# Performance work log

Measured on AMD Instinct MI355X. Metric: run time of the kernel, lower is better.

## Reference

```python
import jax, jax.numpy as jnp
import numpy as np

B, S, D, H, DK, DV = 4, 2048, 512, 8, 64, 64

def setup_inputs() -> dict:
    key = jax.random.key(0)
    ks = jax.random.split(key, 8)
    q = jax.random.normal(ks[0], (B, S, D), dtype=jnp.float32)
    k = jax.random.normal(ks[1], (B, S, D), dtype=jnp.float32)
    v = jax.random.normal(ks[2], (B, S, D), dtype=jnp.float32)
    mask = jax.random.uniform(ks[3], (B, 1, S, S), dtype=jnp.float32)
    sc = 1.0 / np.sqrt(D)
    Wq = jax.random.normal(ks[4], (D, H * DK), dtype=jnp.float32) * sc
    Wk = jax.random.normal(ks[5], (D, H * DK), dtype=jnp.float32) * sc
    Wv = jax.random.normal(ks[6], (D, H * DV), dtype=jnp.float32) * sc
    gamma = jnp.asarray(100.0, dtype=jnp.float32)
    return {"q": q, "k": k, "v": v, "mask": mask, "Wq": Wq, "Wk": Wk, "Wv": Wv, "gamma": gamma}

def reference(q, k, v, mask, Wq, Wk, Wv, gamma):
    temperature = jnp.asarray(DK ** 0.5, dtype=q.dtype)
    # project and split heads: [B,S,H,dk] -> [B,H,S,dk]
    qh = (q @ Wq).reshape(B, S, H, DK).transpose(0, 2, 1, 3)
    kh = (k @ Wk).reshape(B, S, H, DK).transpose(0, 2, 1, 3)
    vh = (v @ Wv).reshape(B, S, H, DV).transpose(0, 2, 1, 3)
    # scores [B,H,S,S] with learnable gamma-scaled additive mask
    scores = jnp.einsum('bhqd,bhkd->bhqk', qh / temperature, kh)
    scores = scores + mask * gamma
    attn = jax.nn.softmax(scores, axis=-1)  # dropout is identity in eval
    out = jnp.einsum('bhqk,bhkd->bhqd', attn, vh)
    out = out.transpose(0, 2, 1, 3).reshape(B, S, H * DV)
    return (out, attn)
```

## Files before the change

kernel.cpp:

```cpp
#include <hip/hip_runtime.h>

typedef __attribute__((ext_vector_type(8))) short short8;
typedef __attribute__((ext_vector_type(4))) float f32x4;

__device__ __forceinline__ short f2bf(float f) {
  union { float f; unsigned u; } x; x.f = f;
  return (short)((x.u + 0x7FFFu + ((x.u >> 16) & 1u)) >> 16);
}
__device__ __forceinline__ unsigned pk2(float a, float b) {
  return (unsigned)(unsigned short)f2bf(a) | ((unsigned)(unsigned short)f2bf(b) << 16);
}
__device__ __forceinline__ float bfu2f(unsigned lo16) {
  union { unsigned u; float f; } x; x.u = lo16 << 16; return x.f;
}

__global__ __launch_bounds__(256) void prep_wt_k(const float* __restrict__ Wq,
    const float* __restrict__ Wk, const float* __restrict__ Wv,
    short* __restrict__ wt) {
  int idx = blockIdx.x * 256 + threadIdx.x;
  int m = idx >> 18;
  int r = idx & 0x3FFFF;
  int k = r >> 9, n = r & 511;
  const float* W = (m == 0) ? Wq : (m == 1) ? Wk : Wv;
  wt[(m << 18) + (n << 9) + k] = f2bf(W[(k << 9) + n]);
}

__global__ __launch_bounds__(256) void xcvt_k(const float* __restrict__ q,
    const float* __restrict__ k_, const float* __restrict__ v,
    short* __restrict__ xb) {
  int i = blockIdx.x * 256 + threadIdx.x;
  int m = i >> 19;
  int r = i & 0x7FFFF;
  const float* X = (m == 0) ? q : (m == 1) ? k_ : v;
  float4 f0 = ((const float4*)X)[2 * r];
  float4 f1 = ((const float4*)X)[2 * r + 1];
  short8 t;
  t[0] = f2bf(f0.x); t[1] = f2bf(f0.y); t[2] = f2bf(f0.z); t[3] = f2bf(f0.w);
  t[4] = f2bf(f1.x); t[5] = f2bf(f1.y); t[6] = f2bf(f1.z); t[7] = f2bf(f1.w);
  *(short8*)(xb + (size_t)i * 8) = t;
}

template<int BF>
__global__ __launch_bounds__(64) void proj_k(const float* __restrict__ q,
    const float* __restrict__ k_, const float* __restrict__ v,
    const short* __restrict__ xb, const short* __restrict__ wt,
    short* __restrict__ qh, short* __restrict__ kh, short* __restrict__ vt) {
  int bid = blockIdx.x;
  int mat = bid >> 10;
  int t = bid & 1023;
  int tm = t >> 3, tn = t & 7;
  const float* X = (mat == 0) ? q : (mat == 1) ? k_ : v;
  const short* Xb = xb + ((size_t)mat << 22);
  const short* W = wt + ((size_t)mat << 18);
  int lane = threadIdx.x;
  int lr = lane & 15, lg = lane >> 4;
  int m0 = tm << 6, n0 = tn << 6;
  f32x4 acc[4][4];
  #pragma unroll
  for (int i = 0; i < 4; i++)
    #pragma unroll
    for (int j = 0; j < 4; j++) acc[i][j] = (f32x4){0.f, 0.f, 0.f, 0.f};
  for (int k0 = 0; k0 < 512; k0 += 32) {
    short8 a[4], bfr[4];
    #pragma unroll
    for (int i = 0; i < 4; i++) {
      if (BF) {
        a[i] = *(const short8*)(Xb + (size_t)(m0 + 16 * i + lr) * 512 + k0 + 8 * lg);
      } else {
        const float* p = X + (size_t)(m0 + 16 * i + lr) * 512 + k0 + 8 * lg;
        float4 f0 = *(const float4*)p;
        float4 f1 = *(const float4*)(p + 4);
        short8 tt;
        tt[0] = f2bf(f0.x); tt[1] = f2bf(f0.y); tt[2] = f2bf(f0.z); tt[3] = f2bf(f0.w);
        tt[4] = f2bf(f1.x); tt[5] = f2bf(f1.y); tt[6] = f2bf(f1.z); tt[7] = f2bf(f1.w);
        a[i] = tt;
      }
    }
    #pragma unroll
    for (int j = 0; j < 4; j++)
      bfr[j] = *(const short8*)(W + (size_t)(n0 + 16 * j + lr) * 512 + k0 + 8 * lg);
    #pragma unroll
    for (int i = 0; i < 4; i++)
      #pragma unroll
      for (int j = 0; j < 4; j++)
        acc[i][j] = __builtin_amdgcn_mfma_f32_16x16x32_bf16(a[i], bfr[j], acc[i][j], 0, 0, 0);
  }
  #pragma unroll
  for (int i = 0; i < 4; i++)
    #pragma unroll
    for (int j = 0; j < 4; j++)
      #pragma unroll
      for (int r = 0; r < 4; r++) {
        int row = m0 + 16 * i + lg * 4 + r;
        int col = n0 + 16 * j + lr;
        int bb = row >> 11, s = row & 2047;
        int h = col >> 6, d = col & 63;
        short val = f2bf(acc[i][j][r]);
        if (mat == 0) {
          qh[((size_t)((bb * 8 + h) * 2048 + s) << 6) + d] = val;
        } else if (mat == 1) {
          int o = s & 31, aa = o >> 3, b7 = o & 7;
          int loc = (b7 < 4) ? ((aa << 2) | b7) : (16 + ((aa << 2) | (b7 - 4)));
          int sp = (s & ~31) | loc;
          kh[((size_t)((bb * 8 + h) * 2048 + sp) << 6) + d] = val;
        } else {
          vt[((size_t)((bb * 8 + h) * 64 + d) << 11) + s] = val;
        }
      }
}

__device__ __forceinline__ float eterm(float s, float m, float cs, float gl2, float sh2) {
  return __builtin_amdgcn_exp2f(fmaf(s, cs, fmaf(m, gl2, -sh2)));
}

__global__ __launch_bounds__(512, 4) void attn_k(const short* __restrict__ qh,
    const short* __restrict__ kh, const short* __restrict__ vt,
    const float* __restrict__ mask, const float* __restrict__ gamma_p,
    float* __restrict__ out, float* __restrict__ attn_out) {
  __shared__ __align__(16) short Kl[2][4096];
  __shared__ __align__(16) short Vl[2][4096];
  __shared__ __align__(16) short P_lds[8][16][64];

  int bid = blockIdx.x;
  int work = ((bid & 7) << 6) + (bid >> 3);
  int bh = work >> 4;
  int qt = work & 15;
  int q0 = qt << 7;
  int bb = bh >> 3, h = bh & 7;
  int tid = threadIdx.x;
  int w = tid >> 6, lane = tid & 63, lr = lane & 15, lg = lane >> 4;
  int qw = q0 + (w << 4);
  int qg = qw + lr;

  const short* Kb = kh + (size_t)bh * (2048 * 64);
  const short* Qb = qh + (size_t)bh * (2048 * 64);
  const short* Vb = vt + (size_t)bh * (64 * 2048);
  const float* Mrow = mask + (size_t)bb * (2048 * 2048) + (size_t)qg * 2048 + (lg << 3);
  float* Ah = attn_out + (size_t)bh * (2048 * 2048);

  const float LOG2E = 1.4426950408889634f;
  float gamma = gamma_p[0];
  float shift = fmaxf(gamma, 0.f) + 16.0f;
  float cs = 0.125f * LOG2E;
  float gl2 = gamma * LOG2E;
  float sh2 = shift * LOG2E;

  int sr = tid >> 3;
  int sb = (tid & 7) << 4;
  int sdst = sr * 64 + (((sb) ^ ((sr & 7) << 4)) >> 1);
  const short* Kg = Kb + (size_t)tid * 8;
  const short* Vg = Vb + (size_t)sr * 2048 + ((tid & 7) << 3);

  short8 qf0 = *(const short8*)(Qb + (size_t)qg * 64 + 8 * lg);
  short8 qf1 = *(const short8*)(Qb + (size_t)qg * 64 + 32 + 8 * lg);
  int sw = lr & 7;

  #define LDK(cu, row, boff) (*(const short8*)&Kl[cu][(row) * 64 + ((((boff) ^ (((row) & 7) << 4))) >> 1)])
  #define LDV(cu, row, boff) (*(const short8*)&Vl[cu][(row) * 64 + ((((boff) ^ (((row) & 7) << 4))) >> 1)])

  float lsum = 0.f;
  {
    short8 ck = *(const short8*)(Kg);
    float4 a0 = *(const float4*)(Mrow + 0);
    float4 a1 = *(const float4*)(Mrow + 4);
    float4 a2 = *(const float4*)(Mrow + 32);
    float4 a3 = *(const float4*)(Mrow + 36);
    *(short8*)&Kl[0][sdst] = ck;
    __syncthreads();
    for (int t = 0; t < 32; ++t) {
      int cu = t & 1, nx = cu ^ 1;
      short8 nk;
      if (t < 31) nk = *(const short8*)(Kg + (size_t)(t + 1) * 4096);
      int nc = ((t + 1) << 6) & 2047;
      float4 n0 = *(const float4*)(Mrow + nc);
      float4 n1 = *(const float4*)(Mrow + nc + 4);
      float4 n2 = *(const float4*)(Mrow + nc + 32);
      float4 n3 = *(const float4*)(Mrow + nc + 36);
      #pragma unroll
      for (int m = 0; m < 2; ++m) {
        int rA = (m << 5) + lr, rC = rA + 16;
        short8 kA = LDK(cu, rA, (lg << 4));
        short8 kB = LDK(cu, rA, 64 + (lg << 4));
        short8 kC = LDK(cu, rC, (lg << 4));
        short8 kD = LDK(cu, rC, 64 + (lg << 4));
        f32x4 s0 = (f32x4){0.f, 0.f, 0.f, 0.f};
        s0 = __builtin_amdgcn_mfma_f32_16x16x32_bf16(kA, qf0, s0, 0, 0, 0);
        s0 = __builtin_amdgcn_mfma_f32_16x16x32_bf16(kB, qf1, s0, 0, 0, 0);
        f32x4 s1 = (f32x4){0.f, 0.f, 0.f, 0.f};
        s1 = __builtin_amdgcn_mfma_f32_16x16x32_bf16(kC, qf0, s1, 0, 0, 0);
        s1 = __builtin_amdgcn_mfma_f32_16x16x32_bf16(kD, qf1, s1, 0, 0, 0);
        float4 ca0 = (m == 0) ? a0 : a2;
        float4 ca1 = (m == 0) ? a1 : a3;
        lsum += eterm(s0[0], ca0.x, cs, gl2, sh2);
        lsum += eterm(s0[1], ca0.y, cs, gl2, sh2);
        lsum += eterm(s0[2], ca0.z, cs, gl2, sh2);
        lsum += eterm(s0[3], ca0.w, cs, gl2, sh2);
        lsum += eterm(s1[0], ca1.x, cs, gl2, sh2);
        lsum += eterm(s1[1], ca1.y, cs, gl2, sh2);
        lsum += eterm(s1[2], ca1.z, cs, gl2, sh2);
        lsum += eterm(s1[3], ca1.w, cs, gl2, sh2);
      }
      if (t < 31) *(short8*)&Kl[nx][sdst] = nk;
      __syncthreads();
      a0 = n0; a1 = n1; a2 = n2; a3 = n3;
    }
  }
  lsum += __shfl_xor(lsum, 16);
  lsum += __shfl_xor(lsum, 32);
  float inv = 1.0f / lsum;

  f32x4 oacc[4];
  #pragma unroll
  for (int j = 0; j < 4; j++) oacc[j] = (f32x4){0.f, 0.f, 0.f, 0.f};

  {
    short8 ck = *(const short8*)(Kg);
    short8 cv = *(const short8*)(Vg);
    float4 a0 = *(const float4*)(Mrow + 0);
    float4 a1 = *(const float4*)(Mrow + 4);
    float4 a2 = *(const float4*)(Mrow + 32);
    float4 a3 = *(const float4*)(Mrow + 36);
    *(short8*)&Kl[0][sdst] = ck;
    *(short8*)&Vl[0][sdst] = cv;
    __syncthreads();
    for (int t = 0; t < 32; ++t) {
      int cu = t & 1, nx = cu ^ 1;
      short8 nk, nv;
      if (t < 31) {
        nk = *(const short8*)(Kg + (size_t)(t + 1) * 4096);
        nv = *(const short8*)(Vg + (size_t)(t + 1) * 64);
      }
      int nc = ((t + 1) << 6) & 2047;
      float4 n0 = *(const float4*)(Mrow + nc);
      float4 n1 = *(const float4*)(Mrow + nc + 4);
      float4 n2 = *(const float4*)(Mrow + nc + 32);
      float4 n3 = *(const float4*)(Mrow + nc + 36);
      #pragma unroll
      for (int m = 0; m < 2; ++m) {
        int rA = (m << 5) + lr, rC = rA + 16;
        short8 kA = LDK(cu, rA, (lg << 4));
        short8 kB = LDK(cu, rA, 64 + (lg << 4));
        short8 kC = LDK(cu, rC, (lg << 4));
        short8 kD = LDK(cu, rC, 64 + (lg << 4));
        short8 v0 = LDV(cu, lr,      (m << 6) + (lg << 4));
        short8 v1 = LDV(cu, 16 + lr, (m << 6) + (lg << 4));
        short8 v2 = LDV(cu, 32 + lr, (m << 6) + (lg << 4));
        short8 v3 = LDV(cu, 48 + lr, (m << 6) + (lg << 4));
        f32x4 s0 = (f32x4){0.f, 0.f, 0.f, 0.f};
        s0 = __builtin_amdgcn_mfma_f32_16x16x32_bf16(kA, qf0, s0, 0, 0, 0);
        s0 = __builtin_amdgcn_mfma_f32_16x16x32_bf16(kB, qf1, s0, 0, 0, 0);
        f32x4 s1 = (f32x4){0.f, 0.f, 0.f, 0.f};
        s1 = __builtin_amdgcn_mfma_f32_16x16x32_bf16(kC, qf0, s1, 0, 0, 0);
        s1 = __builtin_amdgcn_mfma_f32_16x16x32_bf16(kD, qf1, s1, 0, 0, 0);
        float4 ca0 = (m == 0) ? a0 : a2;
        float4 ca1 = (m == 0) ? a1 : a3;
        float p00 = eterm(s0[0], ca0.x, cs, gl2, sh2) * inv;
        float p01 = eterm(s0[1], ca0.y, cs, gl2, sh2) * inv;
        float p02 = eterm(s0[2], ca0.z, cs, gl2, sh2) * inv;
        float p03 = eterm(s0[3], ca0.w, cs, gl2, sh2) * inv;
        float p10 = eterm(s1[0], ca1.x, cs, gl2, sh2) * inv;
        float p11 = eterm(s1[1], ca1.y, cs, gl2, sh2) * inv;
        float p12 = eterm(s1[2], ca1.z, cs, gl2, sh2) * inv;
        float p13 = eterm(s1[3], ca1.w, cs, gl2, sh2) * inv;
        union { unsigned u4[4]; short8 s8; uint4 q4; } pu;
        pu.u4[0] = pk2(p00, p01);
        pu.u4[1] = pk2(p02, p03);
        pu.u4[2] = pk2(p10, p11);
        pu.u4[3] = pk2(p12, p13);
        {
          int c16 = (m << 2) + lg;
          *(uint4*)&P_lds[w][lr][(c16 ^ sw) << 3] = pu.q4;
        }
        oacc[0] = __builtin_amdgcn_mfma_f32_16x16x32_bf16(pu.s8, v0, oacc[0], 0, 0, 0);
        oacc[1] = __builtin_amdgcn_mfma_f32_16x16x32_bf16(pu.s8, v1, oacc[1], 0, 0, 0);
        oacc[2] = __builtin_amdgcn_mfma_f32_16x16x32_bf16(pu.s8, v2, oacc[2], 0, 0, 0);
        oacc[3] = __builtin_amdgcn_mfma_f32_16x16x32_bf16(pu.s8, v3, oacc[3], 0, 0, 0);
      }
      asm volatile("s_waitcnt lgkmcnt(0)" ::: "memory");
      __builtin_amdgcn_sched_barrier(0);
      {
        int fr = lane >> 3;
        int c8 = lane & 7;
        #pragma unroll
        for (int p = 0; p < 2; ++p) {
          int row = fr + (p << 3);
          int unit = c8 ^ (row & 7);
          uint4 pv = *(const uint4*)&P_lds[w][row][unit << 3];
          f32x4 lo = (f32x4){bfu2f(pv.x & 0xFFFFu), bfu2f(pv.x >> 16),
                             bfu2f(pv.y & 0xFFFFu), bfu2f(pv.y >> 16)};
          f32x4 hi = (f32x4){bfu2f(pv.z & 0xFFFFu), bfu2f(pv.z >> 16),
                             bfu2f(pv.w & 0xFFFFu), bfu2f(pv.w >> 16)};
          float* dst = Ah + (size_t)(qw + row) * 2048 + (t << 6) + (c8 << 3);
          *(f32x4*)dst = lo;
          *(f32x4*)(dst + 4) = hi;
        }
      }
      if (t < 31) {
        *(short8*)&Kl[nx][sdst] = nk;
        *(short8*)&Vl[nx][sdst] = nv;
      }
      __syncthreads();
      a0 = n0; a1 = n1; a2 = n2; a3 = n3;
    }
  }

  #pragma unroll
  for (int j = 0; j < 4; j++)
    #pragma unroll
    for (int r = 0; r < 4; r++) {
      int qq = qw + (lg << 2) + r;
      out[((size_t)(bb * 2048) + qq) * 512 + (h << 6) + (j << 4) + lr] = oacc[j][r];
    }
  #undef LDK
  #undef LDV
}

extern "C" void kernel_launch(void* const* d_in, const int* in_sizes, int n_in,
                              void* d_out, int out_size, void* d_ws, size_t ws_size,
                              hipStream_t stream) {
  const float* q    = (const float*)d_in[0];
  const float* k    = (const float*)d_in[1];
  const float* v    = (const float*)d_in[2];
  const float* mask = (const float*)d_in[3];
  const float* Wq   = (const float*)d_in[4];
  const float* Wk   = (const float*)d_in[5];
  const float* Wv   = (const float*)d_in[6];
  const float* gma  = (const float*)d_in[7];
  float* out = (float*)d_out;
  float* attn_out = out + (size_t)4 * 2048 * 512;

  short* wt = (short*)d_ws;
  short* qh = (short*)((char*)d_ws + (2u << 20));
  short* kh = qh + (size_t)4 * 8 * 2048 * 64;
  short* vt = kh + (size_t)4 * 8 * 2048 * 64;
  short* xb = vt + (size_t)4 * 8 * 2048 * 64;
  bool big_ws = ws_size >= (size_t)(50u << 20);

  hipLaunchKernelGGL(prep_wt_k, dim3(3072), dim3(256), 0, stream, Wq, Wk, Wv, wt);
  if (big_ws) {
    hipLaunchKernelGGL(xcvt_k, dim3(6144), dim3(256), 0, stream, q, k, v, xb);
    hipLaunchKernelGGL(proj_k<1>, dim3(3072), dim3(64), 0, stream, q, k, v, xb, wt, qh, kh, vt);
  } else {
    hipLaunchKernelGGL(proj_k<0>, dim3(3072), dim3(64), 0, stream, q, k, v, xb, wt, qh, kh, vt);
  }
  hipLaunchKernelGGL(attn_k, dim3(512), dim3(512), 0, stream, qh, kh, vt, mask, gma,
                     out, attn_out);
}
```

Measured before the change: 346.2 us.

## Deepen K/V prefetch and defer attn-tile writeback via double-buffered P staging

Global K/V loads are now issued two tiles ahead, and each prefetched tile is written to LDS at the top of the next iteration instead of after compute. The P tile staged in LDS is double-buffered, so the attention-probability writeback of tile t-1 happens at the start of iteration t. This removes the explicit lgkmcnt wait and sched barrier that sat between the MFMAs and the store. The aim is to overlap global load latency and the large attn output stores with MFMA work. The cost is another 16KB of LDS for P, which may reduce occupancy at 4 blocks per CU, plus a longer register live range for the prefetched data.

```diff
diff --git a/kernel.cpp b/kernel.cpp
--- a/kernel.cpp
+++ b/kernel.cpp
@@ -119,7 +119,7 @@
     float* __restrict__ out, float* __restrict__ attn_out) {
   __shared__ __align__(16) short Kl[2][4096];
   __shared__ __align__(16) short Vl[2][4096];
-  __shared__ __align__(16) short P_lds[8][16][64];
+  __shared__ __align__(16) short P_lds[2][8][16][64];
 
   int bid = blockIdx.x;
   int work = ((bid & 7) << 6) + (bid >> 3);
@@ -160,22 +160,23 @@
 
   float lsum = 0.f;
   {
-    short8 ck = *(const short8*)(Kg);
+    short8 rk = *(const short8*)(Kg);
+    *(short8*)&Kl[0][sdst] = rk;
+    rk = *(const short8*)(Kg + 4096);
     float4 a0 = *(const float4*)(Mrow + 0);
     float4 a1 = *(const float4*)(Mrow + 4);
     float4 a2 = *(const float4*)(Mrow + 32);
     float4 a3 = *(const float4*)(Mrow + 36);
-    *(short8*)&Kl[0][sdst] = ck;
     __syncthreads();
     for (int t = 0; t < 32; ++t) {
       int cu = t & 1, nx = cu ^ 1;
-      short8 nk;
-      if (t < 31) nk = *(const short8*)(Kg + (size_t)(t + 1) * 4096);
       int nc = ((t + 1) << 6) & 2047;
       float4 n0 = *(const float4*)(Mrow + nc);
       float4 n1 = *(const float4*)(Mrow + nc + 4);
       float4 n2 = *(const float4*)(Mrow + nc + 32);
       float4 n3 = *(const float4*)(Mrow + nc + 36);
+      if (t < 31) *(short8*)&Kl[nx][sdst] = rk;
+      if (t < 30) rk = *(const short8*)(Kg + (size_t)(t + 2) * 4096);
       #pragma unroll
       for (int m = 0; m < 2; ++m) {
         int rA = (m << 5) + lr, rC = rA + 16;
@@ -200,9 +201,8 @@
         lsum += eterm(s1[2], ca1.z, cs, gl2, sh2);
         lsum += eterm(s1[3], ca1.w, cs, gl2, sh2);
       }
-      if (t < 31) *(short8*)&Kl[nx][sdst] = nk;
+      a0 = n0; a1 = n1; a2 = n2; a3 = n3;
       __syncthreads();
-      a0 = n0; a1 = n1; a2 = n2; a3 = n3;
     }
   }
   lsum += __shfl_xor(lsum, 16);
@@ -214,27 +214,49 @@
   for (int j = 0; j < 4; j++) oacc[j] = (f32x4){0.f, 0.f, 0.f, 0.f};
 
   {
-    short8 ck = *(const short8*)(Kg);
-    short8 cv = *(const short8*)(Vg);
+    short8 rk = *(const short8*)(Kg);
+    short8 rv = *(const short8*)(Vg);
+    *(short8*)&Kl[0][sdst] = rk;
+    *(short8*)&Vl[0][sdst] = rv;
+    rk = *(const short8*)(Kg + 4096);
+    rv = *(const short8*)(Vg + 64);
     float4 a0 = *(const float4*)(Mrow + 0);
     float4 a1 = *(const float4*)(Mrow + 4);
     float4 a2 = *(const float4*)(Mrow + 32);
     float4 a3 = *(const float4*)(Mrow + 36);
-    *(short8*)&Kl[0][sdst] = ck;
-    *(short8*)&Vl[0][sdst] = cv;
     __syncthreads();
     for (int t = 0; t < 32; ++t) {
       int cu = t & 1, nx = cu ^ 1;
-      short8 nk, nv;
-      if (t < 31) {
-        nk = *(const short8*)(Kg + (size_t)(t + 1) * 4096);
-        nv = *(const short8*)(Vg + (size_t)(t + 1) * 64);
+      if (t > 0) {
+        int pb = nx;
+        int fr = lane >> 3, c8 = lane & 7;
+        #pragma unroll
+        for (int p = 0; p < 2; ++p) {
+          int row = fr + (p << 3);
+          int unit = c8 ^ (row & 7);
+          uint4 pv = *(const uint4*)&P_lds[pb][w][row][unit << 3];
+          f32x4 lo = (f32x4){bfu2f(pv.x & 0xFFFFu), bfu2f(pv.x >> 16),
+                             bfu2f(pv.y & 0xFFFFu), bfu2f(pv.y >> 16)};
+          f32x4 hi = (f32x4){bfu2f(pv.z & 0xFFFFu), bfu2f(pv.z >> 16),
+                             bfu2f(pv.w & 0xFFFFu), bfu2f(pv.w >> 16)};
+          float* dst = Ah + (size_t)(qw + row) * 2048 + ((t - 1) << 6) + (c8 << 3);
+          *(f32x4*)dst = lo;
+          *(f32x4*)(dst + 4) = hi;
+        }
       }
       int nc = ((t + 1) << 6) & 2047;
       float4 n0 = *(const float4*)(Mrow + nc);
       float4 n1 = *(const float4*)(Mrow + nc + 4);
       float4 n2 = *(const float4*)(Mrow + nc + 32);
       float4 n3 = *(const float4*)(Mrow + nc + 36);
+      if (t < 31) {
+        *(short8*)&Kl[nx][sdst] = rk;
+        *(short8*)&Vl[nx][sdst] = rv;
+      }
+      if (t < 30) {
+        rk = *(const short8*)(Kg + (size_t)(t + 2) * 4096);
+        rv = *(const short8*)(Vg + (size_t)(t + 2) * 64);
+      }
       #pragma unroll
       for (int m = 0; m < 2; ++m) {
         int rA = (m << 5) + lr, rC = rA + 16;
@@ -269,38 +291,31 @@
         pu.u4[3] = pk2(p12, p13);
         {
           int c16 = (m << 2) + lg;
-          *(uint4*)&P_lds[w][lr][(c16 ^ sw) << 3] = pu.q4;
+          *(uint4*)&P_lds[cu][w][lr][(c16 ^ sw) << 3] = pu.q4;
         }
         oacc[0] = __builtin_amdgcn_mfma_f32_16x16x32_bf16(pu.s8, v0, oacc[0], 0, 0, 0);
         oacc[1] = __builtin_amdgcn_mfma_f32_16x16x32_bf16(pu.s8, v1, oacc[1], 0, 0, 0);
         oacc[2] = __builtin_amdgcn_mfma_f32_16x16x32_bf16(pu.s8, v2, oacc[2], 0, 0, 0);
         oacc[3] = __builtin_amdgcn_mfma_f32_16x16x32_bf16(pu.s8, v3, oacc[3], 0, 0, 0);
       }
-      asm volatile("s_waitcnt lgkmcnt(0)" ::: "memory");
-      __builtin_amdgcn_sched_barrier(0);
-      {
-        int fr = lane >> 3;
-        int c8 = lane & 7;
-        #pragma unroll
-        for (int p = 0; p < 2; ++p) {
-          int row = fr + (p << 3);
-          int unit = c8 ^ (row & 7);
-          uint4 pv = *(const uint4*)&P_lds[w][row][unit << 3];
-          f32x4 lo = (f32x4){bfu2f(pv.x & 0xFFFFu), bfu2f(pv.x >> 16),
-                             bfu2f(pv.y & 0xFFFFu), bfu2f(pv.y >> 16)};
-          f32x4 hi = (f32x4){bfu2f(pv.z & 0xFFFFu), bfu2f(pv.z >> 16),
-                             bfu2f(pv.w & 0xFFFFu), bfu2f(pv.w >> 16)};
-          float* dst = Ah + (size_t)(qw + row) * 2048 + (t << 6) + (c8 << 3);
-          *(f32x4*)dst = lo;
-          *(f32x4*)(dst + 4) = hi;
-        }
-      }
-      if (t < 31) {
-        *(short8*)&Kl[nx][sdst] = nk;
-        *(short8*)&Vl[nx][sdst] = nv;
-      }
+      a0 = n0; a1 = n1; a2 = n2; a3 = n3;
       __syncthreads();
-      a0 = n0; a1 = n1; a2 = n2; a3 = n3;
+    }
+    {
+      int fr = lane >> 3, c8 = lane & 7;
+      #pragma unroll
+      for (int p = 0; p < 2; ++p) {
+        int row = fr + (p << 3);
+        int unit = c8 ^ (row & 7);
+        uint4 pv = *(const uint4*)&P_lds[1][w][row][unit << 3];
+        f32x4 lo = (f32x4){bfu2f(pv.x & 0xFFFFu), bfu2f(pv.x >> 16),
+                           bfu2f(pv.y & 0xFFFFu), bfu2f(pv.y >> 16)};
+        f32x4 hi = (f32x4){bfu2f(pv.z & 0xFFFFu), bfu2f(pv.z >> 16),
+                           bfu2f(pv.w & 0xFFFFu), bfu2f(pv.w >> 16)};
+        float* dst = Ah + (size_t)(qw + row) * 2048 + (31 << 6) + (c8 << 3);
+        *(f32x4*)dst = lo;
+        *(f32x4*)(dst + 4) = hi;
+      }
     }
   }
 
```

Result: no change. 349.6 us (+1.0%).
